# Kernel tuning notes

Hardware: AMD Instinct MI355X
Metric: run time of the kernel (lower is better)

Reference implementation:

```python
import jax, jax.numpy as jnp
import numpy as np

C = 256
R = 16  # reduction
CR = C // R
LN_EPS = 1e-5


def setup_inputs() -> dict:
    key = jax.random.key(0)
    ks = jax.random.split(key, 8)
    B, H, W = 16, 128, 128
    x = jax.random.normal(ks[0], (B, C, H, W), dtype=jnp.float32)
    # conv_mask: Conv2d(C, 1, 1x1)
    w_mask = jax.random.normal(ks[1], (C,), dtype=jnp.float32) * (1.0 / np.sqrt(C))
    b_mask = jnp.zeros((), dtype=jnp.float32)
    # channel_add[0]: Conv2d(C, C//R, 1x1)
    w1 = jax.random.normal(ks[2], (CR, C), dtype=jnp.float32) * (1.0 / np.sqrt(C))
    b1 = jnp.zeros((CR,), dtype=jnp.float32)
    # channel_add[1]: LayerNorm([C//R, 1, 1])
    ln_g = jnp.ones((CR,), dtype=jnp.float32)
    ln_b = jnp.zeros((CR,), dtype=jnp.float32)
    # channel_add[3]: Conv2d(C//R, C, 1x1)
    w2 = jax.random.normal(ks[3], (C, CR), dtype=jnp.float32) * (1.0 / np.sqrt(CR))
    b2 = jnp.zeros((C,), dtype=jnp.float32)
    return {"x": x, "w_mask": w_mask, "b_mask": b_mask,
            "w1": w1, "b1": b1, "ln_g": ln_g, "ln_b": ln_b,
            "w2": w2, "b2": b2}


def reference(x, w_mask, b_mask, w1, b1, ln_g, ln_b, w2, b2):
    B, Cc, H, W = x.shape
    # 1x1 conv to 1 channel -> attention logits over H*W
    logits = jnp.einsum('bchw,c->bhw', x, w_mask) + b_mask          # [B,H,W]
    attn = jax.nn.softmax(logits.reshape(B, H * W), axis=-1)        # [B,HW]
    # attention-pooled global context: [B,C]
    context = jnp.einsum('bchw,bs->bc', x, attn.reshape(B, H, W).reshape(B, H * W)[:, :].reshape(B, H * W)) if False else jnp.einsum('bcs,bs->bc', x.reshape(B, Cc, H * W), attn)
    # channel_add MLP: conv1x1 -> LayerNorm over [C//R] -> ReLU -> conv1x1
    t = jnp.einsum('oc,bc->bo', w1, context) + b1                   # [B,C//R]
    mu = jnp.mean(t, axis=-1, keepdims=True)
    var = jnp.mean((t - mu) ** 2, axis=-1, keepdims=True)
    t = (t - mu) / jnp.sqrt(var + LN_EPS) * ln_g + ln_b
    t = jax.nn.relu(t)
    add = jnp.einsum('oc,bc->bo', w2, t) + b2                       # [B,C]
    return x + add[:, :, None, None]
```

## Files before the change

### kernel.cpp

```cpp
#include <hip/hip_runtime.h>
#include <math.h>

#define CC   256
#define CR   16
#define SB   16384
#define NB   16
#define NCHUNK 64
#define CHSZ  256
#define ST   64
#define NT   (SB/ST)
#define LN_EPS 1e-5f

typedef float          vfloat4  __attribute__((ext_vector_type(4)));
typedef unsigned short vushort4 __attribute__((ext_vector_type(4)));

__device__ __forceinline__ unsigned short f2b(float f) {
    unsigned int u;
    __builtin_memcpy(&u, &f, 4);
    unsigned int lsb = (u >> 16) & 1u;
    u += 0x7fffu + lsb;
    return (unsigned short)(u >> 16);
}
__device__ __forceinline__ float b2f(unsigned short u) {
    unsigned int v = ((unsigned int)u) << 16;
    float f;
    __builtin_memcpy(&f, &v, 4);
    return f;
}

__global__ __launch_bounds__(256) void k1_shadow_part(const float* __restrict__ x,
                                                      const float* __restrict__ w_mask,
                                                      unsigned short* __restrict__ shadow,
                                                      float* __restrict__ part) {
    const int t   = threadIdx.x;
    const int bid = blockIdx.x;
    const int sq  = bid & 15;
    const int cg  = (bid >> 4) & 15;
    const int b   = bid >> 8;

    __shared__ float wm[16];
    if (t < 16) wm[t] = w_mask[cg * 16 + t];
    __syncthreads();

    const size_t xbase = ((size_t)b * CC + cg * 16) * SB + sq * 1024 + t * 4;

    vfloat4 v[16];
#pragma unroll
    for (int c = 0; c < 16; ++c)
        v[c] = *reinterpret_cast<const vfloat4*>(x + xbase + (size_t)c * SB);

    float ax = 0.f, ay = 0.f, az = 0.f, aw = 0.f;
#pragma unroll
    for (int c = 0; c < 16; ++c) {
        const float w = wm[c];
        ax += w * v[c].x; ay += w * v[c].y; az += w * v[c].z; aw += w * v[c].w;
    }

    unsigned short* chunk = shadow + (size_t)bid * 16384 + t * 4;
#pragma unroll
    for (int c = 0; c < 16; ++c) {
        vushort4 u = { f2b(v[c].x), f2b(v[c].y), f2b(v[c].z), f2b(v[c].w) };
        *reinterpret_cast<vushort4*>(chunk + c * 1024) = u;
    }
    vfloat4 acc = { ax, ay, az, aw };
    *reinterpret_cast<vfloat4*>(part + ((size_t)b * 16 + cg) * SB + sq * 1024 + t * 4) = acc;
}

__global__ __launch_bounds__(256) void k2_chunks(const float* __restrict__ part,
                                                 float* __restrict__ pl_num,
                                                 float* __restrict__ pm,
                                                 float* __restrict__ ps) {
    const int t  = threadIdx.x;
    const int b  = blockIdx.x >> 6;
    const int ch = blockIdx.x & 63;
    __shared__ float red[256];

    const int s = ch * CHSZ + t;
    float l = 0.f;
#pragma unroll
    for (int cg = 0; cg < 16; ++cg)
        l += part[((size_t)b * 16 + cg) * SB + s];

    red[t] = l; __syncthreads();
    for (int st = 128; st > 0; st >>= 1) {
        if (t < st) red[t] = fmaxf(red[t], red[t + st]);
        __syncthreads();
    }
    const float mc = red[0]; __syncthreads();

    const float p = __expf(l - mc);
    pl_num[(size_t)b * SB + s] = p;

    red[t] = p; __syncthreads();
    for (int st = 128; st > 0; st >>= 1) {
        if (t < st) red[t] += red[t + st];
        __syncthreads();
    }
    if (t == 0) { pm[b * NCHUNK + ch] = mc; ps[b * NCHUNK + ch] = red[0]; }
}

__global__ __launch_bounds__(256) void k3_context(const unsigned short* __restrict__ shadow,
                                                  const float* __restrict__ pl_num,
                                                  const float* __restrict__ pm,
                                                  const float* __restrict__ ps,
                                                  float* __restrict__ ctxp) {
    const int t   = threadIdx.x;
    const int bid = blockIdx.x;
    const int sq  = bid & 15;
    const int cg  = (bid >> 4) & 15;
    const int b   = bid >> 8;

    __shared__ float fxs[4];
    __shared__ float wred[4][16];

    if (t < NCHUNK) {
        const float m_t = pm[b * NCHUNK + t];
        float M = m_t;
#pragma unroll
        for (int off = 32; off > 0; off >>= 1)
            M = fmaxf(M, __shfl_xor(M, off));
        const float f = __expf(m_t - M);
        float z = ps[b * NCHUNK + t] * f;
#pragma unroll
        for (int off = 32; off > 0; off >>= 1)
            z += __shfl_xor(z, off);
        const int rel = t - sq * 4;
        if (rel >= 0 && rel < 4) fxs[rel] = f / z;
    }
    __syncthreads();

    const unsigned short* chunk = shadow + (size_t)bid * 16384;
    float4 p = *reinterpret_cast<const float4*>(pl_num + (size_t)b * SB + sq * 1024 + t * 4);
    const float f = fxs[t >> 6];
    p.x *= f; p.y *= f; p.z *= f; p.w *= f;

    float acc[16];
#pragma unroll
    for (int c = 0; c < 16; ++c) {
        const ushort4 u = *reinterpret_cast<const ushort4*>(chunk + c * 1024 + t * 4);
        acc[c] = b2f(u.x) * p.x + b2f(u.y) * p.y + b2f(u.z) * p.z + b2f(u.w) * p.w;
    }
#pragma unroll
    for (int c = 0; c < 16; ++c) {
#pragma unroll
        for (int off = 32; off > 0; off >>= 1)
            acc[c] += __shfl_xor(acc[c], off);
    }
    const int wv = t >> 6;
    if ((t & 63) == 0) {
#pragma unroll
        for (int c = 0; c < 16; ++c) wred[wv][c] = acc[c];
    }
    __syncthreads();
    if (t < 16)
        ctxp[(size_t)bid * 16 + t] = wred[0][t] + wred[1][t] + wred[2][t] + wred[3][t];
}

__global__ __launch_bounds__(256) void k4_mlp(const float* __restrict__ ctxp,
                                              const float* __restrict__ w1,
                                              const float* __restrict__ b1,
                                              const float* __restrict__ ln_g,
                                              const float* __restrict__ ln_b,
                                              const float* __restrict__ w2,
                                              const float* __restrict__ b2,
                                              float* __restrict__ add) {
    const int b = blockIdx.x;
    const int t = threadIdx.x;
    __shared__ float cx[CC];
    __shared__ float tbuf[CR];
    __shared__ float tn[CR];

    {
        const int cg = t >> 4, c = t & 15;
        float s = 0.f;
#pragma unroll
        for (int sq = 0; sq < 16; ++sq)
            s += ctxp[(((size_t)b * 16 + cg) * 16 + sq) * 16 + c];
        cx[t] = s;
    }
    __syncthreads();

    if (t < CR) {
        float a = b1[t];
        const float* w1r = w1 + (size_t)t * CC;
#pragma unroll 8
        for (int c = 0; c < CC; ++c) a += w1r[c] * cx[c];
        tbuf[t] = a;
    }
    __syncthreads();
    if (t == 0) {
        float mu = 0.f;
        for (int q = 0; q < CR; ++q) mu += tbuf[q];
        mu *= (1.0f / CR);
        float var = 0.f;
        for (int q = 0; q < CR; ++q) { const float d = tbuf[q] - mu; var += d * d; }
        var *= (1.0f / CR);
        const float inv = rsqrtf(var + LN_EPS);
        for (int q = 0; q < CR; ++q) {
            const float v = (tbuf[q] - mu) * inv * ln_g[q] + ln_b[q];
            tn[q] = v > 0.f ? v : 0.f;
        }
    }
    __syncthreads();

    float a = b2[t];
    const float* w2r = w2 + (size_t)t * CR;
#pragma unroll
    for (int o = 0; o < CR; ++o) a += w2r[o] * tn[o];
    add[(size_t)b * CC + t] = a;
}

__global__ __launch_bounds__(256) void k5_add(const unsigned short* __restrict__ shadow,
                                              const float* __restrict__ add,
                                              float* __restrict__ out) {
    const int t   = threadIdx.x;
    const int bid = blockIdx.x;
    const int sq  = bid & 15;
    const int cg  = (bid >> 4) & 15;
    const int b   = bid >> 8;

    __shared__ float adds[16];
    if (t < 16) adds[t] = add[(size_t)b * CC + cg * 16 + t];
    __syncthreads();

    const unsigned short* chunk = shadow + (size_t)bid * 16384 + t * 4;
    ushort4 u[16];
#pragma unroll
    for (int c = 0; c < 16; ++c)
        u[c] = *reinterpret_cast<const ushort4*>(chunk + c * 1024);

    float* ob = out + ((size_t)b * CC + cg * 16) * SB + sq * 1024 + t * 4;
#pragma unroll
    for (int c = 0; c < 16; ++c) {
        const float a = adds[c];
        vfloat4 o = { b2f(u[c].x) + a, b2f(u[c].y) + a, b2f(u[c].z) + a, b2f(u[c].w) + a };
        __builtin_nontemporal_store(o, reinterpret_cast<vfloat4*>(ob + (size_t)c * SB));
    }
}

__global__ __launch_bounds__(256) void f_ctx_partial(const float* __restrict__ x,
                                                     const float* __restrict__ w_mask,
                                                     float* __restrict__ pc,
                                                     float* __restrict__ pm,
                                                     float* __restrict__ ps) {
    __shared__ float plog[ST * 5];
    __shared__ float pl[ST];
    __shared__ float wm[CC];
    __shared__ float red2[CC * 17];

    const int t   = threadIdx.x;
    const int bid = blockIdx.x;
    const int b   = bid / NT;
    const int s0  = (bid % NT) * ST;

    wm[t] = w_mask[t];
    __syncthreads();

    const int g  = t >> 4;
    const int i  = t & 15;
    const int s4 = i << 2;

    const float* xb = x + (size_t)b * CC * SB + s0 + s4;
    float4 v[16];
    float4 acc = make_float4(0.f, 0.f, 0.f, 0.f);
#pragma unroll
    for (int k = 0; k < 16; ++k) {
        const int c = g + (k << 4);
        v[k] = *reinterpret_cast<const float4*>(xb + (size_t)c * SB);
        const float w = wm[c];
        acc.x += v[k].x * w; acc.y += v[k].y * w;
        acc.z += v[k].z * w; acc.w += v[k].w * w;
    }
    acc.x += __shfl_xor(acc.x, 16); acc.y += __shfl_xor(acc.y, 16);
    acc.z += __shfl_xor(acc.z, 16); acc.w += __shfl_xor(acc.w, 16);
    acc.x += __shfl_xor(acc.x, 32); acc.y += __shfl_xor(acc.y, 32);
    acc.z += __shfl_xor(acc.z, 32); acc.w += __shfl_xor(acc.w, 32);
    const int wv = t >> 6;
    if ((t & 63) < 16) {
        plog[(s4 + 0) * 5 + wv] = acc.x;
        plog[(s4 + 1) * 5 + wv] = acc.y;
        plog[(s4 + 2) * 5 + wv] = acc.z;
        plog[(s4 + 3) * 5 + wv] = acc.w;
    }
    __syncthreads();

    if (t < ST) {
        const float logit = plog[t * 5 + 0] + plog[t * 5 + 1]
                          + plog[t * 5 + 2] + plog[t * 5 + 3];
        float m = logit;
#pragma unroll
        for (int off = 32; off > 0; off >>= 1)
            m = fmaxf(m, __shfl_xor(m, off));
        const float p = __expf(logit - m);
        pl[t] = p;
        float sum = p;
#pragma unroll
        for (int off = 32; off > 0; off >>= 1)
            sum += __shfl_xor(sum, off);
        if (t == 0) { pm[bid] = m; ps[bid] = sum; }
    }
    __syncthreads();

    const float p0 = pl[s4 + 0], p1 = pl[s4 + 1];
    const float p2 = pl[s4 + 2], p3 = pl[s4 + 3];
#pragma unroll
    for (int k = 0; k < 16; ++k) {
        const int c = g + (k << 4);
        red2[c * 17 + i] = v[k].x * p0 + v[k].y * p1 + v[k].z * p2 + v[k].w * p3;
    }
    __syncthreads();
    float s = 0.f;
#pragma unroll
    for (int j = 0; j < 16; ++j) s += red2[t * 17 + j];
    pc[(size_t)bid * CC + t] = s;
}

__global__ __launch_bounds__(256) void f_combine_mlp(const float* __restrict__ pc,
                                                     const float* __restrict__ pm,
                                                     const float* __restrict__ ps,
                                                     const float* __restrict__ w1,
                                                     const float* __restrict__ b1,
                                                     const float* __restrict__ ln_g,
                                                     const float* __restrict__ ln_b,
                                                     const float* __restrict__ w2,
                                                     const float* __restrict__ b2,
                                                     float* __restrict__ add) {
    const int b = blockIdx.x;
    const int t = threadIdx.x;
    __shared__ float red[256];
    __shared__ float fx[NT];
    __shared__ float ctx[CC];
    __shared__ float tbuf[CR];
    __shared__ float tn[CR];

    const float m_t = pm[b * NT + t];
    red[t] = m_t; __syncthreads();
    for (int st = 128; st > 0; st >>= 1) {
        if (t < st) red[t] = fmaxf(red[t], red[t + st]);
        __syncthreads();
    }
    const float M = red[0]; __syncthreads();

    const float f = __expf(m_t - M);
    fx[t] = f;
    red[t] = ps[b * NT + t] * f; __syncthreads();
    for (int st = 128; st > 0; st >>= 1) {
        if (t < st) red[t] += red[t + st];
        __syncthreads();
    }
    const float invZ = 1.0f / red[0]; __syncthreads();

    float acc = 0.f;
#pragma unroll 4
    for (int j = 0; j < NT; ++j)
        acc += pc[((size_t)b * NT + j) * CC + t] * fx[j];
    ctx[t] = acc * invZ;
    __syncthreads();

    if (t < CR) {
        float a = b1[t];
        const float* w1r = w1 + (size_t)t * CC;
#pragma unroll 8
        for (int c = 0; c < CC; ++c) a += w1r[c] * ctx[c];
        tbuf[t] = a;
    }
    __syncthreads();
    if (t == 0) {
        float mu = 0.f;
        for (int i = 0; i < CR; ++i) mu += tbuf[i];
        mu *= (1.0f / CR);
        float var = 0.f;
        for (int i = 0; i < CR; ++i) { const float d = tbuf[i] - mu; var += d * d; }
        var *= (1.0f / CR);
        const float inv = rsqrtf(var + LN_EPS);
        for (int i = 0; i < CR; ++i) {
            const float v = (tbuf[i] - mu) * inv * ln_g[i] + ln_b[i];
            tn[i] = v > 0.f ? v : 0.f;
        }
    }
    __syncthreads();

    float a = b2[t];
    const float* w2r = w2 + (size_t)t * CR;
#pragma unroll
    for (int o = 0; o < CR; ++o) a += w2r[o] * tn[o];
    add[(size_t)b * CC + t] = a;
}

__global__ __launch_bounds__(256) void f_add(const float* __restrict__ x,
                                             const float* __restrict__ add,
                                             float* __restrict__ out) {
    const size_t idx = ((size_t)blockIdx.x * 256 + threadIdx.x) * 8;
    const size_t bc = idx / SB;
    const float a = add[bc];
    const float4 v0 = *reinterpret_cast<const float4*>(x + idx);
    const float4 v1 = *reinterpret_cast<const float4*>(x + idx + 4);
    vfloat4 o0 = {v0.x + a, v0.y + a, v0.z + a, v0.w + a};
    vfloat4 o1 = {v1.x + a, v1.y + a, v1.z + a, v1.w + a};
    __builtin_nontemporal_store(o0, reinterpret_cast<vfloat4*>(out + idx));
    __builtin_nontemporal_store(o1, reinterpret_cast<vfloat4*>(out + idx + 4));
}

extern "C" void kernel_launch(void* const* d_in, const int* in_sizes, int n_in,
                              void* d_out, int out_size, void* d_ws, size_t ws_size,
                              hipStream_t stream) {
    const float* x      = (const float*)d_in[0];
    const float* w_mask = (const float*)d_in[1];
    const float* w1     = (const float*)d_in[3];
    const float* b1     = (const float*)d_in[4];
    const float* ln_g   = (const float*)d_in[5];
    const float* ln_b   = (const float*)d_in[6];
    const float* w2     = (const float*)d_in[7];
    const float* b2     = (const float*)d_in[8];
    float* out = (float*)d_out;

    const size_t nx = (size_t)NB * CC * SB;
    unsigned short* shadow = (unsigned short*)d_ws;
    float* fbase  = (float*)((char*)d_ws + nx * sizeof(unsigned short));
    float* part   = fbase;
    float* pl_num = part + (size_t)NB * 16 * SB;
    float* pm     = pl_num + (size_t)NB * SB;
    float* ps     = pm + NB * NCHUNK;
    float* ctxp   = ps + NB * NCHUNK;
    float* add    = ctxp + (size_t)NB * 16 * 16 * 16;
    const size_t need = (size_t)((char*)(add + (size_t)NB * CC) - (char*)d_ws);

    if (ws_size >= need) {
        k1_shadow_part<<<dim3(4096), dim3(256), 0, stream>>>(x, w_mask, shadow, part);
        k2_chunks<<<dim3(NB * NCHUNK), dim3(256), 0, stream>>>(part, pl_num, pm, ps);
        k3_context<<<dim3(4096), dim3(256), 0, stream>>>(shadow, pl_num, pm, ps, ctxp);
        k4_mlp<<<dim3(NB), dim3(256), 0, stream>>>(ctxp, w1, b1, ln_g, ln_b, w2, b2, add);
        k5_add<<<dim3(4096), dim3(256), 0, stream>>>(shadow, add, out);
    } else {
        float* pc  = (float*)d_ws;
        float* fpm = pc + (size_t)NB * NT * CC;
        float* fps = fpm + (size_t)NB * NT;
        float* fad = fps + (size_t)NB * NT;
        f_ctx_partial<<<dim3(NB * NT), dim3(256), 0, stream>>>(x, w_mask, pc, fpm, fps);
        f_combine_mlp<<<dim3(NB), dim3(256), 0, stream>>>(pc, fpm, fps, w1, b1, ln_g, ln_b, w2, b2, fad);
        f_add<<<dim3(NB * CC * SB / 2048), dim3(256), 0, stream>>>(x, fad, out);
    }
}
```

Before: 175.3 us.

## Use linear shadow layout, 8-channel half-spatial blocks, and flat vectorized add kernel

Stores the bf16 shadow copy in the natural channel-major layout instead of per-block chunks, so the final add kernel becomes a flat grid with 16-byte loads per thread. The logit and context kernels now process 8 channels over half of the spatial range per block, iterating over channels to limit live registers. This doubles the number of partial-logit groups and so the partial buffer traffic, and launches fewer, larger blocks in the first and third kernels.

```diff
diff --git a/kernel.cpp b/kernel.cpp
--- a/kernel.cpp
+++ b/kernel.cpp
@@ -5,6 +5,7 @@
 #define CR   16
 #define SB   16384
 #define NB   16
+#define NG   32
 #define NCHUNK 64
 #define CHSZ  256
 #define ST   64
@@ -28,42 +29,49 @@
     return f;
 }
 
-__global__ __launch_bounds__(256) void k1_shadow_part(const float* __restrict__ x,
+__global__ __launch_bounds__(256) void k1_part_shadow(const float* __restrict__ x,
                                                       const float* __restrict__ w_mask,
                                                       unsigned short* __restrict__ shadow,
                                                       float* __restrict__ part) {
     const int t   = threadIdx.x;
     const int bid = blockIdx.x;
-    const int sq  = bid & 15;
-    const int cg  = (bid >> 4) & 15;
-    const int b   = bid >> 8;
-
-    __shared__ float wm[16];
-    if (t < 16) wm[t] = w_mask[cg * 16 + t];
-    __syncthreads();
-
-    const size_t xbase = ((size_t)b * CC + cg * 16) * SB + sq * 1024 + t * 4;
-
-    vfloat4 v[16];
-#pragma unroll
-    for (int c = 0; c < 16; ++c)
-        v[c] = *reinterpret_cast<const vfloat4*>(x + xbase + (size_t)c * SB);
-
-    float ax = 0.f, ay = 0.f, az = 0.f, aw = 0.f;
-#pragma unroll
-    for (int c = 0; c < 16; ++c) {
+    const int h   = bid & 1;
+    const int g   = (bid >> 1) & (NG - 1);
+    const int b   = bid >> 6;
+
+    __shared__ float wm[8];
+    if (t < 8) wm[t] = w_mask[g * 8 + t];
+    __syncthreads();
+
+    const size_t base = ((size_t)b * CC + g * 8) * SB + h * 8192 + t * 4;
+
+    vfloat4 acc[8];
+#pragma unroll
+    for (int j = 0; j < 8; ++j) acc[j] = (vfloat4){0.f, 0.f, 0.f, 0.f};
+
+#pragma unroll
+    for (int c = 0; c < 8; ++c) {
         const float w = wm[c];
-        ax += w * v[c].x; ay += w * v[c].y; az += w * v[c].z; aw += w * v[c].w;
-    }
-
-    unsigned short* chunk = shadow + (size_t)bid * 16384 + t * 4;
-#pragma unroll
-    for (int c = 0; c < 16; ++c) {
-        vushort4 u = { f2b(v[c].x), f2b(v[c].y), f2b(v[c].z), f2b(v[c].w) };
-        *reinterpret_cast<vushort4*>(chunk + c * 1024) = u;
-    }
-    vfloat4 acc = { ax, ay, az, aw };
-    *reinterpret_cast<vfloat4*>(part + ((size_t)b * 16 + cg) * SB + sq * 1024 + t * 4) = acc;
+        const float* rp = x + base + (size_t)c * SB;
+        vfloat4 v[8];
+#pragma unroll
+        for (int j = 0; j < 8; ++j)
+            v[j] = *reinterpret_cast<const vfloat4*>(rp + j * 1024);
+#pragma unroll
+        for (int j = 0; j < 8; ++j)
+            acc[j] += v[j] * w;
+        unsigned short* sp = shadow + base + (size_t)c * SB;
+#pragma unroll
+        for (int j = 0; j < 8; ++j) {
+            vushort4 u = { f2b(v[j].x), f2b(v[j].y), f2b(v[j].z), f2b(v[j].w) };
+            *reinterpret_cast<vushort4*>(sp + j * 1024) = u;
+        }
+    }
+
+    float* pp = part + ((size_t)b * NG + g) * SB + h * 8192 + t * 4;
+#pragma unroll
+    for (int j = 0; j < 8; ++j)
+        *reinterpret_cast<vfloat4*>(pp + j * 1024) = acc[j];
 }
 
 __global__ __launch_bounds__(256) void k2_chunks(const float* __restrict__ part,
@@ -77,9 +85,9 @@
 
     const int s = ch * CHSZ + t;
     float l = 0.f;
-#pragma unroll
-    for (int cg = 0; cg < 16; ++cg)
-        l += part[((size_t)b * 16 + cg) * SB + s];
+#pragma unroll 8
+    for (int g = 0; g < NG; ++g)
+        l += part[((size_t)b * NG + g) * SB + s];
 
     red[t] = l; __syncthreads();
     for (int st = 128; st > 0; st >>= 1) {
@@ -106,12 +114,12 @@
                                                   float* __restrict__ ctxp) {
     const int t   = threadIdx.x;
     const int bid = blockIdx.x;
-    const int sq  = bid & 15;
-    const int cg  = (bid >> 4) & 15;
-    const int b   = bid >> 8;
-
-    __shared__ float fxs[4];
-    __shared__ float wred[4][16];
+    const int h   = bid & 1;
+    const int g   = (bid >> 1) & (NG - 1);
+    const int b   = bid >> 6;
+
+    __shared__ float fxs[NCHUNK];
+    __shared__ float wred[4][8];
 
     if (t < NCHUNK) {
         const float m_t = pm[b * NCHUNK + t];
@@ -124,24 +132,30 @@
 #pragma unroll
         for (int off = 32; off > 0; off >>= 1)
             z += __shfl_xor(z, off);
-        const int rel = t - sq * 4;
-        if (rel >= 0 && rel < 4) fxs[rel] = f / z;
-    }
-    __syncthreads();
-
-    const unsigned short* chunk = shadow + (size_t)bid * 16384;
-    float4 p = *reinterpret_cast<const float4*>(pl_num + (size_t)b * SB + sq * 1024 + t * 4);
-    const float f = fxs[t >> 6];
-    p.x *= f; p.y *= f; p.z *= f; p.w *= f;
-
-    float acc[16];
-#pragma unroll
-    for (int c = 0; c < 16; ++c) {
-        const ushort4 u = *reinterpret_cast<const ushort4*>(chunk + c * 1024 + t * 4);
-        acc[c] = b2f(u.x) * p.x + b2f(u.y) * p.y + b2f(u.z) * p.z + b2f(u.w) * p.w;
-    }
-#pragma unroll
-    for (int c = 0; c < 16; ++c) {
+        fxs[t] = f / z;
+    }
+    __syncthreads();
+
+    const size_t base = ((size_t)b * CC + g * 8) * SB + h * 8192 + t * 4;
+    const float* pn = pl_num + (size_t)b * SB + h * 8192 + t * 4;
+
+    float acc[8];
+#pragma unroll
+    for (int c = 0; c < 8; ++c) acc[c] = 0.f;
+
+#pragma unroll
+    for (int j = 0; j < 8; ++j) {
+        vfloat4 p = *reinterpret_cast<const vfloat4*>(pn + j * 1024);
+        const float f = fxs[h * 32 + j * 4 + (t >> 6)];
+        p *= f;
+#pragma unroll
+        for (int c = 0; c < 8; ++c) {
+            const ushort4 u = *reinterpret_cast<const ushort4*>(shadow + base + (size_t)c * SB + j * 1024);
+            acc[c] += b2f(u.x) * p.x + b2f(u.y) * p.y + b2f(u.z) * p.z + b2f(u.w) * p.w;
+        }
+    }
+#pragma unroll
+    for (int c = 0; c < 8; ++c) {
 #pragma unroll
         for (int off = 32; off > 0; off >>= 1)
             acc[c] += __shfl_xor(acc[c], off);
@@ -149,11 +163,12 @@
     const int wv = t >> 6;
     if ((t & 63) == 0) {
 #pragma unroll
-        for (int c = 0; c < 16; ++c) wred[wv][c] = acc[c];
-    }
-    __syncthreads();
-    if (t < 16)
-        ctxp[(size_t)bid * 16 + t] = wred[0][t] + wred[1][t] + wred[2][t] + wred[3][t];
+        for (int c = 0; c < 8; ++c) wred[wv][c] = acc[c];
+    }
+    __syncthreads();
+    if (t < 8)
+        ctxp[(((size_t)b * NG + g) * 2 + h) * 8 + t] =
+            wred[0][t] + wred[1][t] + wred[2][t] + wred[3][t];
 }
 
 __global__ __launch_bounds__(256) void k4_mlp(const float* __restrict__ ctxp,
@@ -171,12 +186,9 @@
     __shared__ float tn[CR];
 
     {
-        const int cg = t >> 4, c = t & 15;
-        float s = 0.f;
-#pragma unroll
-        for (int sq = 0; sq < 16; ++sq)
-            s += ctxp[(((size_t)b * 16 + cg) * 16 + sq) * 16 + c];
-        cx[t] = s;
+        const int g = t >> 3, c = t & 7;
+        cx[t] = ctxp[(((size_t)b * NG + g) * 2 + 0) * 8 + c]
+              + ctxp[(((size_t)b * NG + g) * 2 + 1) * 8 + c];
     }
     __syncthreads();
 
@@ -213,29 +225,16 @@
 __global__ __launch_bounds__(256) void k5_add(const unsigned short* __restrict__ shadow,
                                               const float* __restrict__ add,
                                               float* __restrict__ out) {
-    const int t   = threadIdx.x;
-    const int bid = blockIdx.x;
-    const int sq  = bid & 15;
-    const int cg  = (bid >> 4) & 15;
-    const int b   = bid >> 8;
-
-    __shared__ float adds[16];
-    if (t < 16) adds[t] = add[(size_t)b * CC + cg * 16 + t];
-    __syncthreads();
-
-    const unsigned short* chunk = shadow + (size_t)bid * 16384 + t * 4;
-    ushort4 u[16];
-#pragma unroll
-    for (int c = 0; c < 16; ++c)
-        u[c] = *reinterpret_cast<const ushort4*>(chunk + c * 1024);
-
-    float* ob = out + ((size_t)b * CC + cg * 16) * SB + sq * 1024 + t * 4;
-#pragma unroll
-    for (int c = 0; c < 16; ++c) {
-        const float a = adds[c];
-        vfloat4 o = { b2f(u[c].x) + a, b2f(u[c].y) + a, b2f(u[c].z) + a, b2f(u[c].w) + a };
-        __builtin_nontemporal_store(o, reinterpret_cast<vfloat4*>(ob + (size_t)c * SB));
-    }
+    const size_t idx = ((size_t)blockIdx.x * 256 + threadIdx.x) * 8;
+    const size_t bc = idx / SB;
+    const float a = add[bc];
+    const uint4 d = *reinterpret_cast<const uint4*>(shadow + idx);
+    vfloat4 o0 = {b2f(d.x & 0xffffu) + a, b2f(d.x >> 16) + a,
+                  b2f(d.y & 0xffffu) + a, b2f(d.y >> 16) + a};
+    vfloat4 o1 = {b2f(d.z & 0xffffu) + a, b2f(d.z >> 16) + a,
+                  b2f(d.w & 0xffffu) + a, b2f(d.w >> 16) + a};
+    __builtin_nontemporal_store(o0, reinterpret_cast<vfloat4*>(out + idx));
+    __builtin_nontemporal_store(o1, reinterpret_cast<vfloat4*>(out + idx + 4));
 }
 
 __global__ __launch_bounds__(256) void f_ctx_partial(const float* __restrict__ x,
@@ -418,19 +417,19 @@
     unsigned short* shadow = (unsigned short*)d_ws;
     float* fbase  = (float*)((char*)d_ws + nx * sizeof(unsigned short));
     float* part   = fbase;
-    float* pl_num = part + (size_t)NB * 16 * SB;
+    float* pl_num = part + (size_t)NB * NG * SB;
     float* pm     = pl_num + (size_t)NB * SB;
     float* ps     = pm + NB * NCHUNK;
     float* ctxp   = ps + NB * NCHUNK;
-    float* add    = ctxp + (size_t)NB * 16 * 16 * 16;
+    float* add    = ctxp + (size_t)NB * NG * 2 * 8;
     const size_t need = (size_t)((char*)(add + (size_t)NB * CC) - (char*)d_ws);
 
     if (ws_size >= need) {
-        k1_shadow_part<<<dim3(4096), dim3(256), 0, stream>>>(x, w_mask, shadow, part);
+        k1_part_shadow<<<dim3(1024), dim3(256), 0, stream>>>(x, w_mask, shadow, part);
         k2_chunks<<<dim3(NB * NCHUNK), dim3(256), 0, stream>>>(part, pl_num, pm, ps);
-        k3_context<<<dim3(4096), dim3(256), 0, stream>>>(shadow, pl_num, pm, ps, ctxp);
+        k3_context<<<dim3(1024), dim3(256), 0, stream>>>(shadow, pl_num, pm, ps, ctxp);
         k4_mlp<<<dim3(NB), dim3(256), 0, stream>>>(ctxp, w1, b1, ln_g, ln_b, w2, b2, add);
-        k5_add<<<dim3(4096), dim3(256), 0, stream>>>(shadow, add, out);
+        k5_add<<<dim3(32768), dim3(256), 0, stream>>>(shadow, add, out);
     } else {
         float* pc  = (float*)d_ws;
         float* fpm = pc + (size_t)NB * NT * CC;
```

After: 214.1 us. 22.1% more time.
